# Optimization experiments

Measured on AMD Instinct MI355X. Metric: run time of the kernel, lower is better.

The kernel has to match this reference:

```python
import jax, jax.numpy as jnp
import numpy as np

# Faithful RBF layer math:
# dists[n,k] = sum_d relu(sigma[d]) * (x[n,d]-center[k,d])^2  (original builds an NxN
# matrix per center just to take its diagonal; we use the algebraic expansion
# x^2.s - 2 (x*s).c^T + c^2.s which is O(N*K*D) and identical math)
# D2 = 1 - dists * relu(width); concat bias column of ones; out = D2_bias @ relu(W_out)

N, D, K, OUT = 131072, 256, 256, 128

def setup_inputs() -> dict:
    key = jax.random.key(0)
    k1, k2, k3, k4 = jax.random.split(key, 4)
    x = jax.random.normal(k1, (N, D), dtype=jnp.float32)
    # 'uniform' keras initializer ~ U(-0.05, 0.05)
    center = jax.random.uniform(k2, (K, D), minval=-0.05, maxval=0.05, dtype=jnp.float32)
    sigma = jax.random.uniform(k3, (1, D), minval=0.5, maxval=1.0, dtype=jnp.float32)
    width = jnp.ones((1, K), dtype=jnp.float32)
    output_weights = jax.random.uniform(k4, (1 + K, OUT), minval=0.5, maxval=1.0, dtype=jnp.float32)
    return {"x": x, "center": center, "sigma": sigma, "width": width,
            "output_weights": output_weights}

def reference(x, center, sigma, width, output_weights):
    s = jax.nn.relu(sigma[0])                       # [D]
    x2 = (x * x) @ s                                # [N]
    c2 = (center * center) @ s                      # [K]
    cross = (x * s) @ center.T                      # [N,K]
    dists = x2[:, None] - 2.0 * cross + c2[None, :] # [N,K] weighted sq-dists
    D2 = 1.0 - dists * jax.nn.relu(width)           # [N,K]
    ones = jnp.ones((x.shape[0], 1), dtype=x.dtype)
    D2_bias = jnp.concatenate([ones, D2], axis=1)   # [N,1+K]
    return D2_bias @ jax.nn.relu(output_weights)    # [N,OUT]
```

## Files before the change

### kernel.cpp

```cpp
#include <hip/hip_runtime.h>


typedef short  short8 __attribute__((ext_vector_type(8)));
typedef __bf16 bf16x8 __attribute__((ext_vector_type(8)));
typedef float  f32x4  __attribute__((ext_vector_type(4)));

#define N_ 131072
#define D_ 256
#define K_ 256
#define O_ 128


__device__ __forceinline__ unsigned short f2bf_bits(float f) {
  unsigned u = __builtin_bit_cast(unsigned, f);
  u += 0x7fffu + ((u >> 16) & 1u);
  return (unsigned short)(u >> 16);
}

__device__ __forceinline__ float relu(float v) { return v > 0.f ? v : 0.f; }

__global__ __launch_bounds__(256) void rbf_pre(
    const float* __restrict__ center, const float* __restrict__ sigma,
    const float* __restrict__ width,  const float* __restrict__ W,
    short* __restrict__ Mfrag, float* __restrict__ Bo, float* __restrict__ S1)
{
  const int tid = threadIdx.x;
  if (blockIdx.x < 64) {
#pragma unroll
    for (int rep = 0; rep < 2; ++rep) {
      const int e    = blockIdx.x * 512 + rep * 256 + tid;
      const int j    = e & 7;
      const int lane = (e >> 3) & 63;
      const int ot   = (e >> 9) & 7;
      const int ks   = (e >> 12) & 7;
      const int d = ks * 32 + (lane >> 4) * 8 + j;
      const int o = ot * 16 + (lane & 15);
      float acc = 0.f;
      for (int k = 0; k < K_; ++k) {
        const float w  = relu(width[k]);
        const float wr = relu(W[(1 + k) * O_ + o]);
        acc = fmaf(center[k * D_ + d] * w, wr, acc);
      }
      Mfrag[e] = (short)f2bf_bits(acc * relu(sigma[d]));
    }
  } else {
    __shared__ float c2s[K_];
    {
      const int k = tid;
      float acc = 0.f;
      for (int d = 0; d < D_; ++d) {
        const float c = center[k * D_ + d];
        acc = fmaf(c * c, relu(sigma[d]), acc);
      }
      c2s[k] = acc;
    }
    __syncthreads();
    if (tid < O_) {
      const int o = tid;
      float s1 = 0.f, sum = 0.f, c2w = 0.f;
      for (int k = 0; k < K_; ++k) {
        const float w  = relu(width[k]);
        const float wr = relu(W[(1 + k) * O_ + o]);
        s1  = fmaf(w, wr, s1);
        sum += wr;
        c2w = fmaf(c2s[k] * w, wr, c2w);
      }
      Bo[o] = relu(W[o]) + sum - c2w;
      S1[o] = s1;
    }
  }
}

__global__ __launch_bounds__(256) void rbf_main(
    const float* __restrict__ x, const float* __restrict__ sigma,
    const short* __restrict__ Mfrag, const float* __restrict__ Bo,
    const float* __restrict__ S1, float* __restrict__ out)
{
  const int lane = threadIdx.x & 63;
  const int wv   = threadIdx.x >> 6;
  const int m    = lane & 15;
  const int q    = lane >> 4;
  const long rowBase = ((long)blockIdx.x * 4 + wv) * 16;

  const float* xr = x + (rowBase + m) * D_ + q * 8;
  const float* sp = sigma + q * 8;

  bf16x8 a[8];
  float x2p = 0.f;
#pragma unroll
  for (int ks = 0; ks < 8; ++ks) {
    float xv[8], sv[8];
    *(f32x4*)(xv)     = *(const f32x4*)(xr + ks * 32);
    *(f32x4*)(xv + 4) = *(const f32x4*)(xr + ks * 32 + 4);
    *(f32x4*)(sv)     = *(const f32x4*)(sp + ks * 32);
    *(f32x4*)(sv + 4) = *(const f32x4*)(sp + ks * 32 + 4);
    short8 ab;
#pragma unroll
    for (int j = 0; j < 8; ++j) {
      const float s = relu(sv[j]);
      const float v = xv[j];
      x2p = fmaf(s * v, v, x2p);
      ab[j] = (short)f2bf_bits(v);
    }
    a[ks] = __builtin_bit_cast(bf16x8, ab);
  }
  x2p += __shfl_xor(x2p, 16);
  x2p += __shfl_xor(x2p, 32);

  const short8* Mf = (const short8*)Mfrag;
#pragma unroll
  for (int ot = 0; ot < 8; ++ot) {
    f32x4 acc = {0.f, 0.f, 0.f, 0.f};
#pragma unroll
    for (int ks = 0; ks < 8; ++ks) {
      const short8 bs = Mf[(ks * 8 + ot) * 64 + lane];
      acc = __builtin_amdgcn_mfma_f32_16x16x32_bf16(
          a[ks], __builtin_bit_cast(bf16x8, bs), acc, 0, 0, 0);
    }
    const int   o  = ot * 16 + m;
    const float bo = Bo[o];
    const float s1 = S1[o];
    float* op = out + rowBase * O_ + o;
#pragma unroll
    for (int r = 0; r < 4; ++r) {
      const int rr = q * 4 + r;
      const float x2r = __shfl(x2p, rr);
      op[(long)rr * O_] = fmaf(2.f, acc[r], fmaf(-x2r, s1, bo));
    }
  }
}

extern "C" void kernel_launch(void* const* d_in, const int* in_sizes, int n_in,
                              void* d_out, int out_size, void* d_ws, size_t ws_size,
                              hipStream_t stream) {
  (void)in_sizes; (void)n_in; (void)out_size; (void)ws_size;
  const float* x      = (const float*)d_in[0];
  const float* center = (const float*)d_in[1];
  const float* sigma  = (const float*)d_in[2];
  const float* width  = (const float*)d_in[3];
  const float* W      = (const float*)d_in[4];
  float* out = (float*)d_out;

  short* Mfrag = (short*)d_ws;
  float* Bo    = (float*)((char*)d_ws + 65536);
  float* S1    = (float*)((char*)d_ws + 66048);

  hipLaunchKernelGGL(rbf_pre, dim3(65), dim3(256), 0, stream,
                     center, sigma, width, W, Mfrag, Bo, S1);
  hipLaunchKernelGGL(rbf_main, dim3(2048), dim3(256), 0, stream,
                     x, sigma, Mfrag, Bo, S1, out);
}
```

Before: 269.9 us.

## Tile precompute through LDS and process 32 rows per wave in main kernel

The precompute kernel now stages the relu'd width*W products and a slice of the centers in shared memory, so each thread reads from LDS rather than re-reading global memory 256 times per element. The main kernel has each wave handle two 16-row tiles, which reuses every Mfrag fragment load across two MFMAs, hoists the Bo/S1 loads, and issues all x loads up front for more memory parallelism. Output stores become nontemporal, the launch-bounds hint allows 2 blocks per CU, and the grid is halved. In exchange, register pressure rises and fewer blocks are in flight.

```diff
diff --git a/kernel.cpp b/kernel.cpp
--- a/kernel.cpp
+++ b/kernel.cpp
@@ -9,7 +9,6 @@
 #define D_ 256
 #define K_ 256
 #define O_ 128
-
 
 __device__ __forceinline__ unsigned short f2bf_bits(float f) {
   unsigned u = __builtin_bit_cast(unsigned, f);
@@ -26,23 +25,38 @@
 {
   const int tid = threadIdx.x;
   if (blockIdx.x < 64) {
+    const int ot = blockIdx.x & 7;
+    const int ks = blockIdx.x >> 3;
+    __shared__ float ww[K_][16];
+    __shared__ float cen[K_][32];
 #pragma unroll
-    for (int rep = 0; rep < 2; ++rep) {
-      const int e    = blockIdx.x * 512 + rep * 256 + tid;
-      const int j    = e & 7;
-      const int lane = (e >> 3) & 63;
-      const int ot   = (e >> 9) & 7;
-      const int ks   = (e >> 12) & 7;
-      const int d = ks * 32 + (lane >> 4) * 8 + j;
-      const int o = ot * 16 + (lane & 15);
-      float acc = 0.f;
-      for (int k = 0; k < K_; ++k) {
-        const float w  = relu(width[k]);
-        const float wr = relu(W[(1 + k) * O_ + o]);
-        acc = fmaf(center[k * D_ + d] * w, wr, acc);
-      }
-      Mfrag[e] = (short)f2bf_bits(acc * relu(sigma[d]));
+    for (int i = 0; i < 16; ++i) {
+      const int k  = i * 16 + (tid >> 4);
+      const int oc = tid & 15;
+      ww[k][oc] = relu(width[k]) * relu(W[(1 + k) * O_ + ot * 16 + oc]);
     }
+#pragma unroll
+    for (int i = 0; i < 32; ++i) {
+      const int k  = i * 8 + (tid >> 5);
+      const int dc = tid & 31;
+      cen[k][dc] = center[k * D_ + ks * 32 + dc];
+    }
+    __syncthreads();
+    const int j   = tid & 7;
+    const int lf  = tid >> 3;
+    const int oc  = lf & 15;
+    const int dc1 = (lf >> 4) * 8 + j;
+    float a1 = 0.f, a2 = 0.f;
+#pragma unroll 8
+    for (int k = 0; k < K_; ++k) {
+      const float w = ww[k][oc];
+      a1 = fmaf(cen[k][dc1],      w, a1);
+      a2 = fmaf(cen[k][dc1 + 16], w, a2);
+    }
+    const int e1 = blockIdx.x * 512 + tid;
+    const int d1 = ks * 32 + dc1;
+    Mfrag[e1]       = (short)f2bf_bits(a1 * relu(sigma[d1]));
+    Mfrag[e1 + 256] = (short)f2bf_bits(a2 * relu(sigma[d1 + 16]));
   } else {
     __shared__ float c2s[K_];
     {
@@ -71,7 +85,7 @@
   }
 }
 
-__global__ __launch_bounds__(256) void rbf_main(
+__global__ __launch_bounds__(256, 2) void rbf_main(
     const float* __restrict__ x, const float* __restrict__ sigma,
     const short* __restrict__ Mfrag, const float* __restrict__ Bo,
     const float* __restrict__ S1, float* __restrict__ out)
@@ -80,52 +94,81 @@
   const int wv   = threadIdx.x >> 6;
   const int m    = lane & 15;
   const int q    = lane >> 4;
-  const long rowBase = ((long)blockIdx.x * 4 + wv) * 16;
+  const long rowBase = ((long)blockIdx.x * 4 + wv) * 32;
 
-  const float* xr = x + (rowBase + m) * D_ + q * 8;
-  const float* sp = sigma + q * 8;
+  const float* xr0 = x + (rowBase + m) * D_ + q * 8;
+  const float* xr1 = xr0 + 16 * D_;
 
-  bf16x8 a[8];
-  float x2p = 0.f;
+  f32x4 raw0[16], raw1[16];
 #pragma unroll
   for (int ks = 0; ks < 8; ++ks) {
-    float xv[8], sv[8];
-    *(f32x4*)(xv)     = *(const f32x4*)(xr + ks * 32);
-    *(f32x4*)(xv + 4) = *(const f32x4*)(xr + ks * 32 + 4);
+    raw0[ks * 2]     = *(const f32x4*)(xr0 + ks * 32);
+    raw0[ks * 2 + 1] = *(const f32x4*)(xr0 + ks * 32 + 4);
+  }
+#pragma unroll
+  for (int ks = 0; ks < 8; ++ks) {
+    raw1[ks * 2]     = *(const f32x4*)(xr1 + ks * 32);
+    raw1[ks * 2 + 1] = *(const f32x4*)(xr1 + ks * 32 + 4);
+  }
+
+  const float* sp = sigma + q * 8;
+  bf16x8 a0[8], a1[8];
+  float x20 = 0.f, x21 = 0.f;
+#pragma unroll
+  for (int ks = 0; ks < 8; ++ks) {
+    float sv[8], v0[8], v1[8];
     *(f32x4*)(sv)     = *(const f32x4*)(sp + ks * 32);
     *(f32x4*)(sv + 4) = *(const f32x4*)(sp + ks * 32 + 4);
-    short8 ab;
+    *(f32x4*)(v0)     = raw0[ks * 2];
+    *(f32x4*)(v0 + 4) = raw0[ks * 2 + 1];
+    *(f32x4*)(v1)     = raw1[ks * 2];
+    *(f32x4*)(v1 + 4) = raw1[ks * 2 + 1];
+    short8 b0, b1;
 #pragma unroll
-    for (int j = 0; j < 8; ++j) {
-      const float s = relu(sv[j]);
-      const float v = xv[j];
-      x2p = fmaf(s * v, v, x2p);
-      ab[j] = (short)f2bf_bits(v);
+    for (int jj = 0; jj < 8; ++jj) {
+      const float s = relu(sv[jj]);
+      x20 = fmaf(s * v0[jj], v0[jj], x20);
+      x21 = fmaf(s * v1[jj], v1[jj], x21);
+      b0[jj] = (short)f2bf_bits(v0[jj]);
+      b1[jj] = (short)f2bf_bits(v1[jj]);
     }
-    a[ks] = __builtin_bit_cast(bf16x8, ab);
+    a0[ks] = __builtin_bit_cast(bf16x8, b0);
+    a1[ks] = __builtin_bit_cast(bf16x8, b1);
   }
-  x2p += __shfl_xor(x2p, 16);
-  x2p += __shfl_xor(x2p, 32);
+  x20 += __shfl_xor(x20, 16);  x20 += __shfl_xor(x20, 32);
+  x21 += __shfl_xor(x21, 16);  x21 += __shfl_xor(x21, 32);
+
+  float bo[8], s1v[8];
+#pragma unroll
+  for (int ot = 0; ot < 8; ++ot) {
+    bo[ot]  = Bo[ot * 16 + m];
+    s1v[ot] = S1[ot * 16 + m];
+  }
 
   const short8* Mf = (const short8*)Mfrag;
 #pragma unroll
   for (int ot = 0; ot < 8; ++ot) {
-    f32x4 acc = {0.f, 0.f, 0.f, 0.f};
+    f32x4 acc0 = {0.f, 0.f, 0.f, 0.f};
+    f32x4 acc1 = {0.f, 0.f, 0.f, 0.f};
 #pragma unroll
     for (int ks = 0; ks < 8; ++ks) {
       const short8 bs = Mf[(ks * 8 + ot) * 64 + lane];
-      acc = __builtin_amdgcn_mfma_f32_16x16x32_bf16(
-          a[ks], __builtin_bit_cast(bf16x8, bs), acc, 0, 0, 0);
+      const bf16x8 bb = __builtin_bit_cast(bf16x8, bs);
+      acc0 = __builtin_amdgcn_mfma_f32_16x16x32_bf16(a0[ks], bb, acc0, 0, 0, 0);
+      acc1 = __builtin_amdgcn_mfma_f32_16x16x32_bf16(a1[ks], bb, acc1, 0, 0, 0);
     }
-    const int   o  = ot * 16 + m;
-    const float bo = Bo[o];
-    const float s1 = S1[o];
-    float* op = out + rowBase * O_ + o;
+    const int o = ot * 16 + m;
+    float* op0 = out + rowBase * O_ + o;
+    float* op1 = op0 + 16 * O_;
 #pragma unroll
     for (int r = 0; r < 4; ++r) {
       const int rr = q * 4 + r;
-      const float x2r = __shfl(x2p, rr);
-      op[(long)rr * O_] = fmaf(2.f, acc[r], fmaf(-x2r, s1, bo));
+      const float x2r0 = __shfl(x20, rr);
+      const float x2r1 = __shfl(x21, rr);
+      __builtin_nontemporal_store(
+          fmaf(2.f, acc0[r], fmaf(-x2r0, s1v[ot], bo[ot])), op0 + (long)rr * O_);
+      __builtin_nontemporal_store(
+          fmaf(2.f, acc1[r], fmaf(-x2r1, s1v[ot], bo[ot])), op1 + (long)rr * O_);
     }
   }
 }
@@ -147,6 +190,6 @@
 
   hipLaunchKernelGGL(rbf_pre, dim3(65), dim3(256), 0, stream,
                      center, sigma, width, W, Mfrag, Bo, S1);
-  hipLaunchKernelGGL(rbf_main, dim3(2048), dim3(256), 0, stream,
+  hipLaunchKernelGGL(rbf_main, dim3(1024), dim3(256), 0, stream,
                      x, sigma, Mfrag, Bo, S1, out);
 }
```

Result: faster. 260.4 us (-3.5%).
